# Optimization experiments

Hardware: AMD Instinct MI355X
Metric: run time of the kernel (lower is better)

## Reference

```python
import jax, jax.numpy as jnp
import numpy as np
import math

L = 4      # model_layers
D = 512    # model_filters
H = 32     # heads = max(D//16, 1)
DH = D // H  # 16
S = 1024   # dataset_dimension == max_len == seq_len
B = 2
EPS = 1e-5


def setup_inputs() -> dict:
    key = jax.random.key(0)
    ks = jax.random.split(key, 12)
    scale = 0.02
    n = lambda k, shape: jax.random.normal(k, shape, dtype=jnp.float32) * scale
    return {
        "x": jax.random.normal(ks[0], (B, S), dtype=jnp.float32),
        "Winit": n(ks[1], (D,)),               # init_linear weight (1->D)
        "binit": jnp.zeros((D,), jnp.float32),
        "Wq": n(ks[2], (L, D, D)), "bq": jnp.zeros((L, D), jnp.float32),
        "Wk": n(ks[3], (L, D, D)), "bk": jnp.zeros((L, D), jnp.float32),
        "Wv": n(ks[4], (L, D, D)), "bv": jnp.zeros((L, D), jnp.float32),
        "Er": jax.random.normal(ks[5], (L, S, DH), dtype=jnp.float32) * scale,
        "Wlin": n(ks[6], (L, D, D)), "blin": jnp.zeros((L, D), jnp.float32),
        "ln_g": jnp.ones((L, D), jnp.float32), "ln_b": jnp.zeros((L, D), jnp.float32),
        "Wout": n(ks[7], (D, 1)),              # output_linear, no bias
    }


def layernorm(x, g, b):
    mu = jnp.mean(x, axis=-1, keepdims=True)
    var = jnp.mean(jnp.square(x - mu), axis=-1, keepdims=True)
    return (x - mu) * jax.lax.rsqrt(var + EPS) * g + b


def rel_attn(h, Wq, bq, Wk, bk, Wv, bv, Er):
    # h: [B, S, D]
    b_, s_, _ = h.shape
    q = (h @ Wq + bq).reshape(b_, s_, H, DH).transpose(0, 2, 1, 3)  # [B,H,S,dh]
    k = (h @ Wk + bk).reshape(b_, s_, H, DH).transpose(0, 2, 1, 3)
    v = (h @ Wv + bv).reshape(b_, s_, H, DH).transpose(0, 2, 1, 3)
    # relative-position term with skew trick (seq_len == max_len -> full Er)
    QEr = jnp.einsum('bhsd,td->bhst', q, Er)                  # [B,H,S,S]
    padded = jnp.pad(QEr, ((0, 0), (0, 0), (0, 0), (1, 0)))   # pad left of last dim
    Srel = padded.reshape(b_, H, s_ + 1, s_)[:, :, 1:, :]     # skew
    scores = (jnp.einsum('bhsd,bhtd->bhst', q, k) + Srel) / math.sqrt(DH)
    mask = jnp.tril(jnp.ones((s_, s_), dtype=bool))           # causal
    scores = jnp.where(mask, scores, -jnp.inf)
    p = jax.nn.softmax(scores, axis=-1)
    o = jnp.einsum('bhst,bhtd->bhsd', p, v)
    return o.transpose(0, 2, 1, 3).reshape(b_, s_, D)


def reference(x, Winit, binit, Wq, bq, Wk, bk, Wv, bv, Er, Wlin, blin, ln_g, ln_b, Wout):
    # init_linear(1->D) on scalar per position, then exact gelu
    h = jax.nn.gelu(x[..., None] * Winit + binit, approximate=False)  # [B,S,D]
    for l in range(L):
        a = rel_attn(h, Wq[l], bq[l], Wk[l], bk[l], Wv[l], bv[l], Er[l])
        y = layernorm(a @ Wlin[l] + blin[l], ln_g[l], ln_b[l])
        h = h + jax.nn.gelu(y, approximate=False)
    return h.sum(axis=-2) @ Wout  # [B,1]
```

## Files before the change

kernel.cpp:

```cpp
#include <hip/hip_runtime.h>
#include <math.h>

#define NL 4
#define DIM 512
#define NH 32
#define DHD 16
#define SEQ 1024
#define NB 2
#define LN_EPS 1e-5f
#define NEGF (-1e30f)
#define QSC 0.36067376022224085f

typedef _Float16 half4 __attribute__((ext_vector_type(4)));
typedef _Float16 half8 __attribute__((ext_vector_type(8)));
typedef float floatx4 __attribute__((ext_vector_type(4)));

__device__ __forceinline__ float gelu_exact(float x) {
    return 0.5f * x * (1.0f + erff(x * 0.70710678118654752f));
}

__device__ __forceinline__ void async16(const void* g, void* l) {
    __builtin_amdgcn_global_load_lds(
        (const __attribute__((address_space(1))) void*)g,
        (__attribute__((address_space(3))) void*)l, 16, 0, 0);
}

__global__ __launch_bounds__(256) void k_prep_all(const float* __restrict__ Wq,
        const float* __restrict__ Wk, const float* __restrict__ Wv,
        const float* __restrict__ Wlin, const float* __restrict__ bq,
        const float* __restrict__ bk, const float* __restrict__ bv,
        const float* __restrict__ Er, const float* __restrict__ x,
        const float* __restrict__ Wi, const float* __restrict__ bi,
        _Float16* __restrict__ Wqkvt, _Float16* __restrict__ Wlint,
        float* __restrict__ bqkv, _Float16* __restrict__ Erh,
        float* __restrict__ h, _Float16* __restrict__ hf) {
    __shared__ _Float16 lt[64][72];
    const int u = blockIdx.x;
    const int tid = threadIdx.x;
    if (u < 1024) {
        const int kx = u & 7, ny = (u >> 3) & 7, mz = u >> 6;
        const int l = mz >> 2, which = mz & 3;
        const float* src = (which == 0) ? Wq : (which == 1) ? Wk : (which == 2) ? Wv : Wlin;
        src += (size_t)l * 262144;
        const float scale = (which == 0) ? QSC : 1.0f;
        _Float16* dst = (which < 3) ? (Wqkvt + (size_t)l * 786432 + (size_t)which * 262144)
                                    : (Wlint + (size_t)l * 262144);
        const int k0 = kx << 6, n0 = ny << 6;
        #pragma unroll
        for (int p = 0; p < 4; p++) {
            int kl = (p << 4) + (tid >> 4);
            int n4 = (tid & 15) << 2;
            float4 wv = *(const float4*)(src + (size_t)(k0 + kl) * 512 + n0 + n4);
            lt[n4 + 0][kl] = (_Float16)(wv.x * scale);
            lt[n4 + 1][kl] = (_Float16)(wv.y * scale);
            lt[n4 + 2][kl] = (_Float16)(wv.z * scale);
            lt[n4 + 3][kl] = (_Float16)(wv.w * scale);
        }
        __syncthreads();
        int nl = tid >> 2, k16 = (tid & 3) << 4;
        float4* d4 = (float4*)(dst + (size_t)(n0 + nl) * 512 + k0 + k16);
        const float4* s4 = (const float4*)&lt[nl][k16];
        d4[0] = s4[0];
        d4[1] = s4[1];
    } else if (u < 2048) {
        int idx0 = ((u - 1024) << 10) + (tid << 2);
        int d = idx0 & 511, bs = idx0 >> 9;
        float xs = x[bs];
        float4 wv = *(const float4*)(Wi + d);
        float4 bv = *(const float4*)(bi + d);
        float4 r;
        r.x = gelu_exact(xs * wv.x + bv.x);
        r.y = gelu_exact(xs * wv.y + bv.y);
        r.z = gelu_exact(xs * wv.z + bv.z);
        r.w = gelu_exact(xs * wv.w + bv.w);
        *(float4*)(h + idx0) = r;
        half4 rh = {(_Float16)r.x, (_Float16)r.y, (_Float16)r.z, (_Float16)r.w};
        *(half4*)(hf + idx0) = rh;
    } else {
        int idx = ((u - 2048) << 8) + tid;
        if (idx < NL * 1536) {
            int l = idx / 1536, j = idx % 1536;
            int which = j >> 9, jj = j & 511;
            float val = (which == 0) ? bq[l * 512 + jj] * QSC
                      : (which == 1) ? bk[l * 512 + jj] : bv[l * 512 + jj];
            bqkv[idx] = val;
        }
        int e = idx - NL * 1536;
        if (e >= 0 && e < NL * SEQ * DHD) Erh[e] = (_Float16)Er[e];
    }
}

__global__ __launch_bounds__(256) void k_gemm_qkv(const _Float16* __restrict__ A,
        const _Float16* __restrict__ Bt, const float* __restrict__ bias,
        _Float16* __restrict__ o16) {
    __shared__ _Float16 As[2 * 64 * 32];
    __shared__ _Float16 Bs[2 * 128 * 32];
    const int tid = threadIdx.x;
    const int w = tid >> 6, lane = tid & 63;
    const int nn = lane & 15, qd = lane >> 4;
    const int wm = (w & 1) << 5, wn = (w >> 1) << 6;
    const int m0 = blockIdx.x << 6, n0 = blockIdx.y << 7;
    const int l2r = lane >> 2, l2c = (lane & 3) << 3;
    const _Float16* Ag = A + (size_t)(m0 + (w << 4) + l2r) * 512 + l2c;
    const _Float16* Bg = Bt + (size_t)(n0 + (w << 5) + l2r) * 512 + l2c;
    _Float16* Al = As + (w << 9);
    _Float16* Bl = Bs + (w << 10);
    floatx4 acc[2][4] = {};
    for (int k0 = 0; k0 < 512; k0 += 64) {
        __syncthreads();
        #pragma unroll
        for (int p = 0; p < 2; p++) {
            async16(Ag + k0 + (p << 5), Al + (p << 11));
            async16(Bg + k0 + (p << 5), Bl + (p << 12));
            async16(Bg + k0 + (p << 5) + (16 << 9), Bl + (p << 12) + (16 << 5));
        }
        __syncthreads();
        #pragma unroll
        for (int ks = 0; ks < 2; ks++) {
            half8 af[2], bf[4];
            #pragma unroll
            for (int t = 0; t < 2; t++)
                af[t] = *(const half8*)&As[(ks << 11) + ((wm + (t << 4) + nn) << 5) + (qd << 3)];
            #pragma unroll
            for (int t = 0; t < 4; t++)
                bf[t] = *(const half8*)&Bs[(ks << 12) + ((wn + (t << 4) + nn) << 5) + (qd << 3)];
            #pragma unroll
            for (int ti = 0; ti < 2; ti++)
                #pragma unroll
                for (int tj = 0; tj < 4; tj++)
                    acc[ti][tj] = __builtin_amdgcn_mfma_f32_16x16x32_f16(
                            af[ti], bf[tj], acc[ti][tj], 0, 0, 0);
        }
    }
    float bv4[4];
    #pragma unroll
    for (int tj = 0; tj < 4; tj++) bv4[tj] = bias[n0 + wn + (tj << 4) + nn];
    #pragma unroll
    for (int ti = 0; ti < 2; ti++) {
        int rowg = m0 + wm + (ti << 4) + (qd << 2);
        #pragma unroll
        for (int tj = 0; tj < 4; tj++) {
            int colg = n0 + wn + (tj << 4) + nn;
            int which = colg >> 9, ci = colg & 511;
            _Float16* op = o16 + (size_t)which * 1048576 + (size_t)rowg * 512 + ci;
            #pragma unroll
            for (int r = 0; r < 4; r++)
                op[(size_t)r * 512] = (_Float16)(acc[ti][tj][r] + bv4[tj]);
        }
    }
}

__global__ __launch_bounds__(256) void k_gemm_lin(const _Float16* __restrict__ A,
        const _Float16* __restrict__ Bt, const float* __restrict__ bias,
        float* __restrict__ y) {
    __shared__ _Float16 As[2 * 64 * 32];
    __shared__ _Float16 Bs[2 * 64 * 32];
    const int tid = threadIdx.x;
    const int w = tid >> 6, lane = tid & 63;
    const int nn = lane & 15, qd = lane >> 4;
    const int wm = (w & 1) << 5, wn = (w >> 1) << 5;
    const int m0 = blockIdx.x << 6, n0 = blockIdx.y << 6;
    const int l2r = lane >> 2, l2c = (lane & 3) << 3;
    const _Float16* Ag = A + (size_t)(m0 + (w << 4) + l2r) * 512 + l2c;
    const _Float16* Bg = Bt + (size_t)(n0 + (w << 4) + l2r) * 512 + l2c;
    _Float16* Al = As + (w << 9);
    _Float16* Bl = Bs + (w << 9);
    floatx4 acc[2][2] = {};
    for (int k0 = 0; k0 < 512; k0 += 64) {
        __syncthreads();
        #pragma unroll
        for (int p = 0; p < 2; p++) {
            async16(Ag + k0 + (p << 5), Al + (p << 11));
            async16(Bg + k0 + (p << 5), Bl + (p << 11));
        }
        __syncthreads();
        #pragma unroll
        for (int ks = 0; ks < 2; ks++) {
            half8 af[2], bf[2];
            #pragma unroll
            for (int t = 0; t < 2; t++) {
                af[t] = *(const half8*)&As[(ks << 11) + ((wm + (t << 4) + nn) << 5) + (qd << 3)];
                bf[t] = *(const half8*)&Bs[(ks << 11) + ((wn + (t << 4) + nn) << 5) + (qd << 3)];
            }
            #pragma unroll
            for (int ti = 0; ti < 2; ti++)
                #pragma unroll
                for (int tj = 0; tj < 2; tj++)
                    acc[ti][tj] = __builtin_amdgcn_mfma_f32_16x16x32_f16(
                            af[ti], bf[tj], acc[ti][tj], 0, 0, 0);
        }
    }
    float bv2[2];
    #pragma unroll
    for (int tj = 0; tj < 2; tj++) bv2[tj] = bias[n0 + wn + (tj << 4) + nn];
    #pragma unroll
    for (int ti = 0; ti < 2; ti++) {
        int rg = m0 + wm + (ti << 4) + (qd << 2);
        #pragma unroll
        for (int tj = 0; tj < 2; tj++) {
            int colg = n0 + wn + (tj << 4) + nn;
            float* op = y + (size_t)rg * 512 + colg;
            #pragma unroll
            for (int r = 0; r < 4; r++)
                op[(size_t)r * 512] = acc[ti][tj][r] + bv2[tj];
        }
    }
}

__global__ __launch_bounds__(256, 4) void k_attn_mfma(const _Float16* __restrict__ q,
        const _Float16* __restrict__ k, const _Float16* __restrict__ v,
        const _Float16* __restrict__ Er, _Float16* __restrict__ aout) {
    __shared__ _Float16 Ks[256][20];
    __shared__ _Float16 Vts[16][268];
    __shared__ float Rel[4][16][80];
    const int tid = threadIdx.x;
    const int wid = tid >> 6, lane = tid & 63;
    const int nn = lane & 15, a4 = (lane >> 4) << 2;
    const int b_ = blockIdx.x >> 5, h_ = blockIdx.x & 31;
    const int y = blockIdx.y;
    const int t_ = tid >> 2, c4 = (tid & 3) << 2;
    const int r0p[2] = {64 * y, 64 * (15 - y)};
    const int R = r0p[1] + 64;

    half4 qf[2];
    floatx4 O[2];
    float m[2], lsum[2];
    #pragma unroll
    for (int ph = 0; ph < 2; ph++) {
        int s0w = r0p[ph] + (wid << 4);
        qf[ph] = *(const half4*)(q + ((size_t)(b_ * SEQ + s0w + nn)) * DIM + h_ * DHD + a4);
        O[ph] = (floatx4){0.f, 0.f, 0.f, 0.f};
        m[ph] = NEGF;
        lsum[ph] = 0.f;
    }

    for (int part = 0; part < 4; part++) {
        const int p0 = part << 8;
        if (p0 >= R) break;
        const int pend = (R < p0 + 256) ? R : (p0 + 256);
        __syncthreads();
        const int ng = (pend - p0) >> 6;
        for (int g = 0; g < ng; g++) {
            int rl = (g << 6) + t_;
            size_t gb = ((size_t)(b_ * SEQ + p0 + rl)) * DIM + h_ * DHD + c4;
            *(half4*)&Ks[rl][c4] = *(const half4*)(k + gb);
            half4 vv4 = *(const half4*)(v + gb);
            Vts[c4 + 0][rl] = vv4.x;
            Vts[c4 + 1][rl] = vv4.y;
            Vts[c4 + 2][rl] = vv4.z;
            Vts[c4 + 3][rl] = vv4.w;
        }
        __syncthreads();
        #pragma unroll
        for (int ph = 0; ph < 2; ph++) {
            const int r0 = r0p[ph];
            const int s0w = r0 + (wid << 4);
            const int hi = (r0 + 64 < pend) ? (r0 + 64) : pend;
            for (int ct = p0; ct < hi; ct += 64) {
                const int ctl = ct - p0;
                const int jbw = 1008 - s0w + ct;
                #pragma unroll
                for (int jt = 0; jt < 5; jt++) {
                    int j = jbw + (jt << 4) + nn;
                    j = (j < SEQ - 1) ? j : (SEQ - 1);
                    half4 ef = *(const half4*)(Er + (size_t)j * DHD + a4);
                    floatx4 racc = {0.f, 0.f, 0.f, 0.f};
                    racc = __builtin_amdgcn_mfma_f32_16x16x16f16(ef, qf[ph], racc, 0, 0, 0);
                    *(floatx4*)&Rel[wid][nn][(jt << 4) + a4] = racc;
                }
                float st[4][4];
                const bool diag = (ct == r0);
                #pragma unroll
                for (int tt = 0; tt < 4; tt++) {
                    half4 kf = *(const half4*)&Ks[ctl + (tt << 4) + nn][a4];
                    floatx4 sacc = {0.f, 0.f, 0.f, 0.f};
                    sacc = __builtin_amdgcn_mfma_f32_16x16x16f16(kf, qf[ph], sacc, 0, 0, 0);
                    #pragma unroll
                    for (int r = 0; r < 4; r++) {
                        int tl = (tt << 4) + a4 + r;
                        float sv = sacc[r] + Rel[wid][nn][15 - nn + tl];
                        if (diag && (tl > (wid << 4) + nn)) sv = NEGF;
                        st[tt][r] = sv;
                    }
                }
                float cmax = NEGF;
                #pragma unroll
                for (int tt = 0; tt < 4; tt++)
                    #pragma unroll
                    for (int r = 0; r < 4; r++) cmax = fmaxf(cmax, st[tt][r]);
                cmax = fmaxf(cmax, __shfl_xor(cmax, 16));
                cmax = fmaxf(cmax, __shfl_xor(cmax, 32));
                float mnew = fmaxf(m[ph], cmax);
                float alpha = exp2f(m[ph] - mnew);
                m[ph] = mnew;
                float csum = 0.f;
                half4 pf[4];
                #pragma unroll
                for (int tt = 0; tt < 4; tt++) {
                    float p0e = exp2f(st[tt][0] - mnew);
                    float p1e = exp2f(st[tt][1] - mnew);
                    float p2e = exp2f(st[tt][2] - mnew);
                    float p3e = exp2f(st[tt][3] - mnew);
                    csum += (p0e + p1e) + (p2e + p3e);
                    half4 ph4 = {(_Float16)p0e, (_Float16)p1e, (_Float16)p2e, (_Float16)p3e};
                    pf[tt] = ph4;
                }
                lsum[ph] = lsum[ph] * alpha + csum;
                O[ph][0] *= alpha; O[ph][1] *= alpha; O[ph][2] *= alpha; O[ph][3] *= alpha;
                #pragma unroll
                for (int tt = 0; tt < 4; tt++) {
                    half4 vf = *(const half4*)&Vts[nn][ctl + (tt << 4) + a4];
                    O[ph] = __builtin_amdgcn_mfma_f32_16x16x16f16(vf, pf[tt], O[ph], 0, 0, 0);
                }
            }
        }
    }
    #pragma unroll
    for (int ph = 0; ph < 2; ph++) {
        float lt = lsum[ph];
        lt += __shfl_xor(lt, 16);
        lt += __shfl_xor(lt, 32);
        float linv = 1.0f / lt;
        int s0w = r0p[ph] + (wid << 4);
        half4 ov = { (_Float16)(O[ph][0] * linv), (_Float16)(O[ph][1] * linv),
                     (_Float16)(O[ph][2] * linv), (_Float16)(O[ph][3] * linv) };
        *(half4*)(aout + ((size_t)(b_ * SEQ + s0w + nn)) * DIM + h_ * DHD + a4) = ov;
    }
}

__global__ __launch_bounds__(256) void k_ln_gelu_res(const float* __restrict__ y,
        const float* __restrict__ gam, const float* __restrict__ bet,
        float* __restrict__ h, _Float16* __restrict__ hf) {
    int row = (blockIdx.x << 2) + (threadIdx.x >> 6);
    int lane = threadIdx.x & 63;
    const float* yr = y + (size_t)row * DIM + (lane << 3);
    float4 v0 = *(const float4*)(yr);
    float4 v1 = *(const float4*)(yr + 4);
    float sum = (v0.x + v0.y) + (v0.z + v0.w) + (v1.x + v1.y) + (v1.z + v1.w);
    float sq = v0.x*v0.x + v0.y*v0.y + v0.z*v0.z + v0.w*v0.w
             + v1.x*v1.x + v1.y*v1.y + v1.z*v1.z + v1.w*v1.w;
    #pragma unroll
    for (int off = 32; off > 0; off >>= 1) {
        sum += __shfl_xor(sum, off);
        sq  += __shfl_xor(sq, off);
    }
    float mu = sum * (1.0f / DIM);
    float var = sq * (1.0f / DIM) - mu * mu;
    float rs = rsqrtf(var + LN_EPS);
    float4 g0 = *(const float4*)(gam + (lane << 3));
    float4 g1 = *(const float4*)(gam + (lane << 3) + 4);
    float4 b0 = *(const float4*)(bet + (lane << 3));
    float4 b1 = *(const float4*)(bet + (lane << 3) + 4);
    float* hr = h + (size_t)row * DIM + (lane << 3);
    float4 h0 = *(const float4*)(hr);
    float4 h1 = *(const float4*)(hr + 4);
    float o[8];
    o[0] = h0.x + gelu_exact((v0.x - mu) * rs * g0.x + b0.x);
    o[1] = h0.y + gelu_exact((v0.y - mu) * rs * g0.y + b0.y);
    o[2] = h0.z + gelu_exact((v0.z - mu) * rs * g0.z + b0.z);
    o[3] = h0.w + gelu_exact((v0.w - mu) * rs * g0.w + b0.w);
    o[4] = h1.x + gelu_exact((v1.x - mu) * rs * g1.x + b1.x);
    o[5] = h1.y + gelu_exact((v1.y - mu) * rs * g1.y + b1.y);
    o[6] = h1.z + gelu_exact((v1.z - mu) * rs * g1.z + b1.z);
    o[7] = h1.w + gelu_exact((v1.w - mu) * rs * g1.w + b1.w);
    *(float4*)(hr)     = make_float4(o[0], o[1], o[2], o[3]);
    *(float4*)(hr + 4) = make_float4(o[4], o[5], o[6], o[7]);
    half8 oh = {(_Float16)o[0], (_Float16)o[1], (_Float16)o[2], (_Float16)o[3],
                (_Float16)o[4], (_Float16)o[5], (_Float16)o[6], (_Float16)o[7]};
    *(half8*)(hf + (size_t)row * DIM + (lane << 3)) = oh;
}

__global__ __launch_bounds__(256) void k_colsum(const float* __restrict__ h,
        float* __restrict__ partial) {
    int bt = blockIdx.x;
    int b_ = bt >> 4, t = bt & 15;
    int tid = threadIdx.x;
    #pragma unroll
    for (int half = 0; half < 2; half++) {
        int d = half * 256 + tid;
        float acc = 0.f;
        for (int i = 0; i < 64; i++)
            acc += h[((size_t)(b_ * SEQ + t * 64 + i)) * DIM + d];
        partial[(size_t)bt * DIM + d] = acc;
    }
}

__global__ __launch_bounds__(256) void k_final(const float* __restrict__ partial,
        const float* __restrict__ Wout, float* __restrict__ out) {
    __shared__ float red[4][2];
    int tid = threadIdx.x;
    float acc0 = 0.f, acc1 = 0.f;
    #pragma unroll
    for (int half = 0; half < 2; half++) {
        int d = half * 256 + tid;
        float w = Wout[d];
        float s0 = 0.f, s1 = 0.f;
        for (int t = 0; t < 16; t++) {
            s0 += partial[t * DIM + d];
            s1 += partial[(16 + t) * DIM + d];
        }
        acc0 += s0 * w;
        acc1 += s1 * w;
    }
    #pragma unroll
    for (int off = 32; off > 0; off >>= 1) {
        acc0 += __shfl_down(acc0, off);
        acc1 += __shfl_down(acc1, off);
    }
    if ((tid & 63) == 0) { red[tid >> 6][0] = acc0; red[tid >> 6][1] = acc1; }
    __syncthreads();
    if (tid == 0) {
        out[0] = red[0][0] + red[1][0] + red[2][0] + red[3][0];
        out[1] = red[0][1] + red[1][1] + red[2][1] + red[3][1];
    }
}

extern "C" void kernel_launch(void* const* d_in, const int* in_sizes, int n_in,
                              void* d_out, int out_size, void* d_ws, size_t ws_size,
                              hipStream_t stream) {
    const float* x    = (const float*)d_in[0];
    const float* Wi   = (const float*)d_in[1];
    const float* bi   = (const float*)d_in[2];
    const float* Wq   = (const float*)d_in[3];
    const float* bq   = (const float*)d_in[4];
    const float* Wk   = (const float*)d_in[5];
    const float* bk   = (const float*)d_in[6];
    const float* Wv   = (const float*)d_in[7];
    const float* bv   = (const float*)d_in[8];
    const float* Er   = (const float*)d_in[9];
    const float* Wlin = (const float*)d_in[10];
    const float* blin = (const float*)d_in[11];
    const float* lng  = (const float*)d_in[12];
    const float* lnb  = (const float*)d_in[13];
    const float* Wout = (const float*)d_in[14];
    float* out = (float*)d_out;

    float* ws = (float*)d_ws;
    const size_t N1 = 1048576;
    float*     h     = ws;
    _Float16*  hf    = (_Float16*)(ws + N1);
    _Float16*  qh    = (_Float16*)(ws + N1 + N1/2);
    _Float16*  ah    = (_Float16*)(ws + 3 * N1);
    float*     y     = ws + 3 * N1 + N1/2;
    _Float16*  Wqkvt = (_Float16*)(ws + 4 * N1 + N1/2);
    _Float16*  Wlint = (_Float16*)(ws + 6 * N1);
    float*     bqkv  = ws + 6 * N1 + N1/2;
    _Float16*  Erh   = (_Float16*)(ws + 6 * N1 + N1/2 + 8192);
    float*     pa    = ws + 6 * N1 + N1/2 + 8192 + 32768;

    k_prep_all<<<dim3(2328), dim3(256), 0, stream>>>(Wq, Wk, Wv, Wlin, bq, bk, bv,
            Er, x, Wi, bi, Wqkvt, Wlint, bqkv, Erh, h, hf);
    for (int l = 0; l < NL; l++) {
        k_gemm_qkv<<<dim3(32, 12), dim3(256), 0, stream>>>(
                hf, Wqkvt + (size_t)l * 786432, bqkv + l * 1536, qh);
        k_attn_mfma<<<dim3(NB * NH, 8), dim3(256), 0, stream>>>(
                qh, qh + 1048576, qh + 2097152, Erh + (size_t)l * 16384, ah);
        k_gemm_lin<<<dim3(32, 8), dim3(256), 0, stream>>>(
                ah, Wlint + (size_t)l * 262144, blin + l * 512, y);
        k_ln_gelu_res<<<dim3(512), dim3(256), 0, stream>>>(
                y, lng + l * 512, lnb + l * 512, h, hf);
    }
    k_colsum<<<dim3(32), dim3(256), 0, stream>>>(h, pa);
    k_final<<<dim3(1), dim3(256), 0, stream>>>(pa, Wout, out);
}
```

Measured before the change: 315.0 us.

## Retile QKV GEMM to 128x96 blocks and split final column sum into two stages

The QKV projection GEMM moves from 64x128 tiles on a 32x12 grid to 128x96 tiles on a 16x16 grid, giving each wave a 64x48 sub-tile with more MFMAs per fragment load and fewer blocks. The final column reduction, previously run by only 32 blocks each looping over 64 rows, is split into a 256-block first pass plus a small second reduction kernel to spread the memory reads across more CUs. The attention kernel also hoists the relative-score pointer out of its inner loop. The trade-offs are higher register pressure per thread in the GEMM, fewer blocks than CUs, and one extra kernel launch at the tail.

```diff
diff --git a/kernel.cpp b/kernel.cpp
--- a/kernel.cpp
+++ b/kernel.cpp
@@ -93,59 +93,65 @@
 __global__ __launch_bounds__(256) void k_gemm_qkv(const _Float16* __restrict__ A,
         const _Float16* __restrict__ Bt, const float* __restrict__ bias,
         _Float16* __restrict__ o16) {
-    __shared__ _Float16 As[2 * 64 * 32];
-    __shared__ _Float16 Bs[2 * 128 * 32];
+    __shared__ _Float16 As[2][128][32];
+    __shared__ _Float16 Bs[2][96][32];
     const int tid = threadIdx.x;
     const int w = tid >> 6, lane = tid & 63;
     const int nn = lane & 15, qd = lane >> 4;
-    const int wm = (w & 1) << 5, wn = (w >> 1) << 6;
-    const int m0 = blockIdx.x << 6, n0 = blockIdx.y << 7;
-    const int l2r = lane >> 2, l2c = (lane & 3) << 3;
-    const _Float16* Ag = A + (size_t)(m0 + (w << 4) + l2r) * 512 + l2c;
-    const _Float16* Bg = Bt + (size_t)(n0 + (w << 5) + l2r) * 512 + l2c;
-    _Float16* Al = As + (w << 9);
-    _Float16* Bl = Bs + (w << 10);
-    floatx4 acc[2][4] = {};
+    const int wm = (w & 1) << 6;
+    const int wn = (w >> 1) * 48;
+    const int m0 = blockIdx.x << 7;
+    const int n0 = blockIdx.y * 96;
+    const int srow = lane >> 2, scol = (lane & 3) << 3;
+    floatx4 acc[4][3] = {};
     for (int k0 = 0; k0 < 512; k0 += 64) {
         __syncthreads();
         #pragma unroll
         for (int p = 0; p < 2; p++) {
-            async16(Ag + k0 + (p << 5), Al + (p << 11));
-            async16(Bg + k0 + (p << 5), Bl + (p << 12));
-            async16(Bg + k0 + (p << 5) + (16 << 9), Bl + (p << 12) + (16 << 5));
+            #pragma unroll
+            for (int hh = 0; hh < 2; hh++)
+                async16(A + (size_t)(m0 + (hh << 6) + (w << 4) + srow) * 512
+                          + k0 + (p << 5) + scol,
+                        &As[p][(hh << 6) + (w << 4)][0]);
+            async16(Bt + (size_t)(n0 + (w << 4) + srow) * 512 + k0 + (p << 5) + scol,
+                    &Bs[p][(w << 4)][0]);
+            if (w < 2)
+                async16(Bt + (size_t)(n0 + 64 + (w << 4) + srow) * 512
+                           + k0 + (p << 5) + scol,
+                        &Bs[p][64 + (w << 4)][0]);
         }
         __syncthreads();
         #pragma unroll
         for (int ks = 0; ks < 2; ks++) {
-            half8 af[2], bf[4];
-            #pragma unroll
-            for (int t = 0; t < 2; t++)
-                af[t] = *(const half8*)&As[(ks << 11) + ((wm + (t << 4) + nn) << 5) + (qd << 3)];
+            half8 af[4], bf[3];
             #pragma unroll
             for (int t = 0; t < 4; t++)
-                bf[t] = *(const half8*)&Bs[(ks << 12) + ((wn + (t << 4) + nn) << 5) + (qd << 3)];
-            #pragma unroll
-            for (int ti = 0; ti < 2; ti++)
-                #pragma unroll
-                for (int tj = 0; tj < 4; tj++)
+                af[t] = *(const half8*)&As[ks][wm + (t << 4) + nn][qd << 3];
+            #pragma unroll
+            for (int t = 0; t < 3; t++)
+                bf[t] = *(const half8*)&Bs[ks][wn + (t << 4) + nn][qd << 3];
+            #pragma unroll
+            for (int ti = 0; ti < 4; ti++)
+                #pragma unroll
+                for (int tj = 0; tj < 3; tj++)
                     acc[ti][tj] = __builtin_amdgcn_mfma_f32_16x16x32_f16(
                             af[ti], bf[tj], acc[ti][tj], 0, 0, 0);
         }
     }
-    float bv4[4];
-    #pragma unroll
-    for (int tj = 0; tj < 4; tj++) bv4[tj] = bias[n0 + wn + (tj << 4) + nn];
-    #pragma unroll
-    for (int ti = 0; ti < 2; ti++) {
-        int rowg = m0 + wm + (ti << 4) + (qd << 2);
-        #pragma unroll
-        for (int tj = 0; tj < 4; tj++) {
+    float bv3[3];
+    #pragma unroll
+    for (int tj = 0; tj < 3; tj++) bv3[tj] = bias[n0 + wn + (tj << 4) + nn];
+    #pragma unroll
+    for (int ti = 0; ti < 4; ti++) {
+        int rg = m0 + wm + (ti << 4) + (qd << 2);
+        #pragma unroll
+        for (int tj = 0; tj < 3; tj++) {
             int colg = n0 + wn + (tj << 4) + nn;
             int which = colg >> 9, ci = colg & 511;
-            _Float16* op = o16 + (size_t)which * 1048576 + (size_t)rowg * 512 + ci;
+            _Float16* op = o16 + (size_t)which * 1048576 + (size_t)rg * 512 + ci;
             #pragma unroll
             for (int r = 0; r < 4; r++)
-                op[(size_t)r * 512] = (_Float16)(acc[ti][tj][r] + bv4[tj]);
+                op[(size_t)r * 512] = (_Float16)(acc[ti][tj][r] + bv3[tj]);
         }
     }
 }
@@ -275,10 +281,11 @@
                     half4 kf = *(const half4*)&Ks[ctl + (tt << 4) + nn][a4];
                     floatx4 sacc = {0.f, 0.f, 0.f, 0.f};
                     sacc = __builtin_amdgcn_mfma_f32_16x16x16f16(kf, qf[ph], sacc, 0, 0, 0);
+                    const float* rp = &Rel[wid][nn][15 - nn + (tt << 4) + a4];
                     #pragma unroll
                     for (int r = 0; r < 4; r++) {
                         int tl = (tt << 4) + a4 + r;
-                        float sv = sacc[r] + Rel[wid][nn][15 - nn + tl];
+                        float sv = sacc[r] + rp[r];
                         if (diag && (tl > (wid << 4) + nn)) sv = NEGF;
                         st[tt][r] = sv;
                     }
@@ -370,37 +377,49 @@
     *(half8*)(hf + (size_t)row * DIM + (lane << 3)) = oh;
 }
 
-__global__ __launch_bounds__(256) void k_colsum(const float* __restrict__ h,
-        float* __restrict__ partial) {
+__global__ __launch_bounds__(256) void k_colsum1(const float* __restrict__ h,
+        float* __restrict__ pa) {
     int bt = blockIdx.x;
-    int b_ = bt >> 4, t = bt & 15;
+    int base = bt << 3;
     int tid = threadIdx.x;
     #pragma unroll
     for (int half = 0; half < 2; half++) {
-        int d = half * 256 + tid;
+        int d = (half << 8) + tid;
         float acc = 0.f;
-        for (int i = 0; i < 64; i++)
-            acc += h[((size_t)(b_ * SEQ + t * 64 + i)) * DIM + d];
-        partial[(size_t)bt * DIM + d] = acc;
-    }
-}
-
-__global__ __launch_bounds__(256) void k_final(const float* __restrict__ partial,
+        #pragma unroll
+        for (int i = 0; i < 8; i++)
+            acc += h[(size_t)(base + i) * DIM + d];
+        pa[(size_t)bt * DIM + d] = acc;
+    }
+}
+
+__global__ __launch_bounds__(256) void k_colsum2(const float* __restrict__ pa,
+        float* __restrict__ pb) {
+    __shared__ float red[4][64];
+    int b = blockIdx.x, dt = blockIdx.y;
+    int tid = threadIdx.x;
+    int c = tid & 63, ig = tid >> 6;
+    int d = (dt << 6) + c;
+    float s = 0.f;
+    for (int i = ig; i < 128; i += 4)
+        s += pa[(size_t)(b * 128 + i) * DIM + d];
+    red[ig][c] = s;
+    __syncthreads();
+    if (ig == 0)
+        pb[(size_t)b * DIM + d] = red[0][c] + red[1][c] + red[2][c] + red[3][c];
+}
+
+__global__ __launch_bounds__(256) void k_final(const float* __restrict__ pb,
         const float* __restrict__ Wout, float* __restrict__ out) {
     __shared__ float red[4][2];
     int tid = threadIdx.x;
     float acc0 = 0.f, acc1 = 0.f;
     #pragma unroll
     for (int half = 0; half < 2; half++) {
-        int d = half * 256 + tid;
+        int d = (half << 8) + tid;
         float w = Wout[d];
-        float s0 = 0.f, s1 = 0.f;
-        for (int t = 0; t < 16; t++) {
-            s0 += partial[t * DIM + d];
-            s1 += partial[(16 + t) * DIM + d];
-        }
-        acc0 += s0 * w;
-        acc1 += s1 * w;
+        acc0 += pb[d] * w;
+        acc1 += pb[DIM + d] * w;
     }
     #pragma unroll
     for (int off = 32; off > 0; off >>= 1) {
@@ -447,11 +466,12 @@
     float*     bqkv  = ws + 6 * N1 + N1/2;
     _Float16*  Erh   = (_Float16*)(ws + 6 * N1 + N1/2 + 8192);
     float*     pa    = ws + 6 * N1 + N1/2 + 8192 + 32768;
+    float*     pb    = pa + 131072;
 
     k_prep_all<<<dim3(2328), dim3(256), 0, stream>>>(Wq, Wk, Wv, Wlin, bq, bk, bv,
             Er, x, Wi, bi, Wqkvt, Wlint, bqkv, Erh, h, hf);
     for (int l = 0; l < NL; l++) {
-        k_gemm_qkv<<<dim3(32, 12), dim3(256), 0, stream>>>(
+        k_gemm_qkv<<<dim3(16, 16), dim3(256), 0, stream>>>(
                 hf, Wqkvt + (size_t)l * 786432, bqkv + l * 1536, qh);
         k_attn_mfma<<<dim3(NB * NH, 8), dim3(256), 0, stream>>>(
                 qh, qh + 1048576, qh + 2097152, Erh + (size_t)l * 16384, ah);
@@ -460,6 +480,7 @@
         k_ln_gelu_res<<<dim3(512), dim3(256), 0, stream>>>(
                 y, lng + l * 512, lnb + l * 512, h, hf);
     }
-    k_colsum<<<dim3(32), dim3(256), 0, stream>>>(h, pa);
-    k_final<<<dim3(1), dim3(256), 0, stream>>>(pa, Wout, out);
-}
+    k_colsum1<<<dim3(256), dim3(256), 0, stream>>>(h, pa);
+    k_colsum2<<<dim3(2, 8), dim3(256), 0, stream>>>(pa, pb);
+    k_final<<<dim3(1), dim3(256), 0, stream>>>(pb, Wout, out);
+}
```

Result: slower. 323.1 us (+2.6%).
